# Kernel optimization log

Hardware: AMD Instinct MI355X
Metric: run time of the kernel (lower is better)

## Reference

```python
import jax, jax.numpy as jnp
import numpy as np

N = 50000      # nodes
E = 800000     # edges (before self loops)
D = 128        # embedding_dimension
HEADS = 4
C = 32         # hidden_channels
NEG_SLOPE = 0.2


def setup_inputs() -> dict:
    key = jax.random.key(0)
    ks = jax.random.split(key, 12)
    s = 0.1
    x = jax.random.normal(ks[0], (N, D), jnp.float32)
    edge_index = jax.random.randint(ks[1], (2, E), 0, N)
    # layer 1: D -> HEADS*C, concat
    W1 = jax.random.normal(ks[2], (D, HEADS * C), jnp.float32) * s
    a_src1 = jax.random.normal(ks[3], (HEADS, C), jnp.float32) * s
    a_dst1 = jax.random.normal(ks[4], (HEADS, C), jnp.float32) * s
    b1 = jnp.zeros((HEADS * C,), jnp.float32)
    # layer 2: HEADS*C -> HEADS*C, concat
    W2 = jax.random.normal(ks[5], (HEADS * C, HEADS * C), jnp.float32) * s
    a_src2 = jax.random.normal(ks[6], (HEADS, C), jnp.float32) * s
    a_dst2 = jax.random.normal(ks[7], (HEADS, C), jnp.float32) * s
    b2 = jnp.zeros((HEADS * C,), jnp.float32)
    # layer 3: HEADS*C -> C, heads=1, no concat (mean over the single head)
    W3 = jax.random.normal(ks[8], (HEADS * C, C), jnp.float32) * s
    a_src3 = jax.random.normal(ks[9], (1, C), jnp.float32) * s
    a_dst3 = jax.random.normal(ks[10], (1, C), jnp.float32) * s
    b3 = jnp.zeros((C,), jnp.float32)
    return {"x": x, "edge_index": edge_index,
            "W1": W1, "a_src1": a_src1, "a_dst1": a_dst1, "b1": b1,
            "W2": W2, "a_src2": a_src2, "a_dst2": a_dst2, "b2": b2,
            "W3": W3, "a_src3": a_src3, "a_dst3": a_dst3, "b3": b3}


def gat_layer(x, src, dst, W, a_s, a_d, b, heads, concat):
    """One PyG-style GATConv (eval mode: dropout inactive).
    x: [N, Fin]; src/dst: [E2] (self loops included)."""
    n = x.shape[0]
    h = (x @ W).reshape(n, heads, -1)                 # [N, H, C]
    alpha_src = (h * a_s).sum(-1)                     # [N, H]
    alpha_dst = (h * a_d).sum(-1)                     # [N, H]
    logits = jax.nn.leaky_relu(alpha_src[src] + alpha_dst[dst], NEG_SLOPE)  # [E2, H]
    # segment softmax over destination nodes
    m = jax.ops.segment_max(logits, dst, num_segments=n)          # [N, H]
    ex = jnp.exp(logits - m[dst])                                  # [E2, H]
    denom = jax.ops.segment_sum(ex, dst, num_segments=n)          # [N, H]
    alpha = ex / (denom[dst] + 1e-16)                              # [E2, H]
    msg = h[src] * alpha[:, :, None]                               # [E2, H, C]
    out = jax.ops.segment_sum(msg, dst, num_segments=n)            # [N, H, C]
    if concat:
        return out.reshape(n, -1) + b
    return out.mean(axis=1) + b


def reference(x, edge_index, W1, a_src1, a_dst1, b1, W2, a_src2, a_dst2, b2,
              W3, a_src3, a_dst3, b3):
    loops = jnp.arange(N, dtype=edge_index.dtype)
    src = jnp.concatenate([edge_index[0], loops])   # add_self_loops=True
    dst = jnp.concatenate([edge_index[1], loops])
    h = gat_layer(x, src, dst, W1, a_src1, a_dst1, b1, HEADS, True)
    h = jax.nn.elu(h)
    h = gat_layer(h, src, dst, W2, a_src2, a_dst2, b2, HEADS, True)
    h = jax.nn.elu(h)
    out = gat_layer(h, src, dst, W3, a_src3, a_dst3, b3, 1, False)
    return out
```

## Files before the change

### kernel.cpp

```cpp
#include <hip/hip_runtime.h>
#include <cmath>

constexpr int NN  = 50000;
constexpr int EE  = 800000;
constexpr int E2C = EE + NN;
constexpr int DIM = 128;

constexpr int NBUCK = 256;
constexpr int BW    = 196;
constexpr int EPT   = 16;
constexpr int CH    = 256 * EPT;
constexpr int NB_B  = (E2C + CH - 1) / CH;
constexpr int CAP   = 4096;

using bf16x8 = __attribute__((ext_vector_type(8))) short;
using f32x4  = __attribute__((ext_vector_type(4))) float;

__device__ inline unsigned bf16rne(float f) {
    unsigned u = __builtin_bit_cast(unsigned, f);
    return (u + 0x7fffu + ((u >> 16) & 1u)) >> 16;
}
__device__ inline float bflo(unsigned u) { return __builtin_bit_cast(float, u << 16); }
__device__ inline float bfhi(unsigned u) { return __builtin_bit_cast(float, u & 0xffff0000u); }

__global__ __launch_bounds__(256) void cvt_weights(
    const float* __restrict__ W1, const float* __restrict__ W2,
    const float* __restrict__ W3,
    unsigned short* __restrict__ W1t, unsigned short* __restrict__ W2t,
    unsigned short* __restrict__ W3t)
{
    int g = blockIdx.x * 256 + threadIdx.x;
    const float* W; unsigned short* Wt; int cols;
    if (g < 2048)      { W = W1; Wt = W1t; cols = 128; }
    else if (g < 4096) { W = W2; Wt = W2t; cols = 128; g -= 2048; }
    else if (g < 4608) { W = W3; Wt = W3t; cols = 32;  g -= 4096; }
    else return;
    int c  = g / 16;
    int k8 = (g % 16) * 8;
    unsigned up[4];
    #pragma unroll
    for (int j = 0; j < 4; ++j) {
        float a = W[(k8 + 2 * j) * cols + c];
        float b = W[(k8 + 2 * j + 1) * cols + c];
        up[j] = bf16rne(a) | (bf16rne(b) << 16);
    }
    uint4 u; u.x = up[0]; u.y = up[1]; u.z = up[2]; u.w = up[3];
    *(uint4*)(Wt + c * 128 + k8) = u;
}

template<int NT, int NH, bool F32IN>
__global__ __launch_bounds__(256) void gemm_mfma(
    const void* __restrict__ inv, const unsigned short* __restrict__ Wt,
    const float* __restrict__ a_s, const float* __restrict__ a_d,
    unsigned short* __restrict__ hout, float* __restrict__ asrc,
    float* __restrict__ adst)
{
    constexpr int COLS = NT * 16;
    constexpr int TPH  = NT / NH;
    const int lane = threadIdx.x & 63;
    const int wave = threadIdx.x >> 6;
    const int m    = lane & 15;
    const int quad = lane >> 4;
    const int n0   = blockIdx.x * 64 + wave * 16;

    int arow = n0 + m; if (arow >= NN) arow = NN - 1;

    f32x4 acc[NT] = {};
    #pragma unroll
    for (int kq = 0; kq < 4; ++kq) {
        bf16x8 a;
        if constexpr (F32IN) {
            const float* ap = (const float*)inv + (long long)arow * 128 + quad * 8 + kq * 32;
            float4 v0 = *(const float4*)ap;
            float4 v1 = *(const float4*)(ap + 4);
            a[0] = (short)bf16rne(v0.x); a[1] = (short)bf16rne(v0.y);
            a[2] = (short)bf16rne(v0.z); a[3] = (short)bf16rne(v0.w);
            a[4] = (short)bf16rne(v1.x); a[5] = (short)bf16rne(v1.y);
            a[6] = (short)bf16rne(v1.z); a[7] = (short)bf16rne(v1.w);
        } else {
            a = *(const bf16x8*)((const unsigned short*)inv
                    + (long long)arow * 128 + quad * 8 + kq * 32);
        }
        #pragma unroll
        for (int t = 0; t < NT; ++t) {
            bf16x8 b = *(const bf16x8*)(Wt + (t * 16 + m) * 128 + kq * 32 + quad * 8);
            acc[t] = __builtin_amdgcn_mfma_f32_16x16x32_bf16(a, b, acc[t], 0, 0, 0);
        }
    }

    #pragma unroll
    for (int r = 0; r < 4; ++r) {
        int node = n0 + quad * 4 + r;
        if (node < NN) {
            #pragma unroll
            for (int t = 0; t < NT; ++t)
                hout[(long long)node * COLS + t * 16 + m] =
                    (unsigned short)bf16rne(acc[t][r]);
        }
    }

    float asv[NT], adv[NT];
    #pragma unroll
    for (int t = 0; t < NT; ++t) { asv[t] = a_s[t * 16 + m]; adv[t] = a_d[t * 16 + m]; }

    #pragma unroll
    for (int r = 0; r < 4; ++r) {
        const int node = n0 + quad * 4 + r;
        #pragma unroll
        for (int hh = 0; hh < NH; ++hh) {
            float ps = 0.f, pd = 0.f;
            #pragma unroll
            for (int q = 0; q < TPH; ++q) {
                int t = hh * TPH + q;
                ps = fmaf(acc[t][r], asv[t], ps);
                pd = fmaf(acc[t][r], adv[t], pd);
            }
            #pragma unroll
            for (int off = 8; off > 0; off >>= 1) {
                ps += __shfl_down(ps, off, 16);
                pd += __shfl_down(pd, off, 16);
            }
            if (m == 0 && node < NN) {
                asrc[node * NH + hh] = ps;
                adst[node * NH + hh] = pd;
            }
        }
    }

    if (blockIdx.x == 0 && threadIdx.x == 0) {
        #pragma unroll
        for (int hh = 0; hh < NH; ++hh) asrc[NN * NH + hh] = -1e30f;
    }
}

__global__ __launch_bounds__(256) void bucket_bin(
    const int* __restrict__ ei, int* __restrict__ bcursor,
    unsigned* __restrict__ pairs)
{
    __shared__ int cnt[NBUCK];
    __shared__ int scanex[NBUCK];
    __shared__ int base[NBUCK];
    __shared__ int cur[NBUCK];
    __shared__ unsigned stage[CH];

    const int tid = threadIdx.x;
    const long long e0 = (long long)blockIdx.x * CH;
    cnt[tid] = 0;
    __syncthreads();

    unsigned rec[EPT]; int bk[EPT];
    #pragma unroll
    for (int j = 0; j < EPT; ++j) {
        long long e = e0 + tid + j * 256;
        bool valid = e < E2C;
        int ss = 0, dd = 0;
        if (valid) {
            if (e < EE) { ss = ei[e]; dd = ei[EE + e]; }
            else        { ss = dd = (int)(e - EE); }
        }
        int b = dd / BW;
        bk[j]  = valid ? b : -1;
        rec[j] = (unsigned)ss | ((unsigned)(dd - b * BW) << 16) | ((unsigned)b << 24);
        if (valid) atomicAdd(&cnt[b], 1);
    }
    __syncthreads();

    const int myc = cnt[tid];
    scanex[tid] = myc;
    __syncthreads();
    for (int off = 1; off < NBUCK; off <<= 1) {
        int t = (tid >= off) ? scanex[tid - off] : 0;
        __syncthreads();
        scanex[tid] += t;
        __syncthreads();
    }
    int excl = scanex[tid] - myc;
    __syncthreads();
    scanex[tid] = excl;
    cur[tid]    = excl;
    base[tid]   = atomicAdd(&bcursor[tid], myc);
    __syncthreads();

    #pragma unroll
    for (int j = 0; j < EPT; ++j) {
        if (bk[j] >= 0) {
            int p = atomicAdd(&cur[bk[j]], 1);
            stage[p] = rec[j];
        }
    }
    __syncthreads();

    const int total = (e0 + CH <= E2C) ? CH : (int)(E2C - e0);
    for (int j = tid; j < total; j += 256) {
        unsigned p = stage[j];
        int b = (int)(p >> 24);
        pairs[(size_t)b * CAP + base[b] + (j - scanex[b])] = p;
    }
}

__global__ __launch_bounds__(256) void bucket_sort(
    const int* __restrict__ bcursor, const unsigned* __restrict__ pairs,
    int* __restrict__ rowptr, unsigned short* __restrict__ sorted_src)
{
    __shared__ int deg[256];
    __shared__ int cur[256];
    __shared__ int gsc[256];
    const int b  = blockIdx.x;
    const int n0 = b * BW;
    const int n1 = (n0 + BW < NN) ? n0 + BW : NN;
    const int nloc = n1 - n0;
    const int tid = threadIdx.x;

    int cb = bcursor[tid];
    gsc[tid] = cb;
    __syncthreads();
    for (int off = 1; off < NBUCK; off <<= 1) {
        int t = (tid >= off) ? gsc[tid - off] : 0;
        __syncthreads();
        gsc[tid] += t;
        __syncthreads();
    }
    const int mycnt = bcursor[b];
    const int beg   = gsc[b] - mycnt;
    const unsigned* seg = pairs + (size_t)b * CAP;

    deg[tid] = 0;
    __syncthreads();
    for (int i = tid; i < mycnt; i += 256)
        atomicAdd(&deg[(seg[i] >> 16) & 0xff], 1);
    __syncthreads();

    int v = deg[tid];
    cur[tid] = v;
    __syncthreads();
    for (int off = 1; off < 256; off <<= 1) {
        int t = (tid >= off) ? cur[tid - off] : 0;
        __syncthreads();
        cur[tid] += t;
        __syncthreads();
    }
    int excl = cur[tid] - v;
    __syncthreads();
    cur[tid] = beg + excl;
    if (tid < nloc) rowptr[n0 + tid] = beg + excl;
    if (b == NBUCK - 1 && tid == 0) rowptr[NN] = E2C;
    __syncthreads();

    for (int i = tid; i < mycnt; i += 256) {
        unsigned p = seg[i];
        int pos = atomicAdd(&cur[(p >> 16) & 0xff], 1);
        sorted_src[pos] = (unsigned short)(p & 0xffff);
    }
}

template<int COLS, int NH, bool DO_ELU, bool OUTBF>
__global__ __launch_bounds__(256) void aggr_csr(
    const int* __restrict__ rowptr, const unsigned short* __restrict__ sorted_src,
    const unsigned short* __restrict__ hin,
    const float* __restrict__ asrc, const float* __restrict__ adst,
    const float* __restrict__ bias, void* __restrict__ outv)
{
    constexpr int TPN = COLS / 8;
    constexpr int USTR = COLS / 2;
    int t = blockIdx.x * 256 + threadIdx.x;
    int d = t / TPN;
    int lc = t % TPN;
    if (d >= NN) return;
    const int cc = lc * 8;
    const int head = cc / 32;
    const float ad = adst[d * NH + head];
    const int beg = rowptr[d], end = rowptr[d + 1];
    const uint* hp = (const uint*)hin + cc / 2;

    float num[8] = {};
    float den = 0.f;

    for (int i = beg; i < end; i += 4) {
        int   s[4];
        float a[4];
        uint4 Hv[4];
        #pragma unroll
        for (int j = 0; j < 4; ++j) {
            int sv = sorted_src[i + j];
            s[j] = (i + j < end) ? sv : NN;
        }
        #pragma unroll
        for (int j = 0; j < 4; ++j) a[j] = asrc[s[j] * NH + head];
        #pragma unroll
        for (int j = 0; j < 4; ++j)
            Hv[j] = *(const uint4*)&hp[(long long)s[j] * USTR];
        #pragma unroll
        for (int j = 0; j < 4; ++j) {
            float l = a[j] + ad; l = l > 0.f ? l : 0.2f * l;
            float w = __builtin_expf(l);
            den += w;
            num[0] = fmaf(w, bflo(Hv[j].x), num[0]); num[1] = fmaf(w, bfhi(Hv[j].x), num[1]);
            num[2] = fmaf(w, bflo(Hv[j].y), num[2]); num[3] = fmaf(w, bfhi(Hv[j].y), num[3]);
            num[4] = fmaf(w, bflo(Hv[j].z), num[4]); num[5] = fmaf(w, bfhi(Hv[j].z), num[5]);
            num[6] = fmaf(w, bflo(Hv[j].w), num[6]); num[7] = fmaf(w, bfhi(Hv[j].w), num[7]);
        }
    }

    float inv = 1.f / (den + 1e-16f);
    float v[8];
    #pragma unroll
    for (int j = 0; j < 8; ++j) {
        v[j] = num[j] * inv + bias[cc + j];
        if (DO_ELU) v[j] = v[j] > 0.f ? v[j] : expm1f(v[j]);
    }
    if constexpr (OUTBF) {
        uint4 u;
        u.x = bf16rne(v[0]) | (bf16rne(v[1]) << 16);
        u.y = bf16rne(v[2]) | (bf16rne(v[3]) << 16);
        u.z = bf16rne(v[4]) | (bf16rne(v[5]) << 16);
        u.w = bf16rne(v[6]) | (bf16rne(v[7]) << 16);
        *(uint4*)((unsigned short*)outv + (long long)d * COLS + cc) = u;
    } else {
        float4 o0 = {v[0], v[1], v[2], v[3]};
        float4 o1 = {v[4], v[5], v[6], v[7]};
        float* out = (float*)outv;
        *(float4*)&out[(long long)d * COLS + cc]     = o0;
        *(float4*)&out[(long long)d * COLS + cc + 4] = o1;
    }
}

extern "C" void kernel_launch(void* const* d_in, const int* in_sizes, int n_in,
                              void* d_out, int out_size, void* d_ws, size_t ws_size,
                              hipStream_t stream)
{
    const float* x   = (const float*)d_in[0];
    const int*   ei  = (const int*)  d_in[1];
    const float* W1  = (const float*)d_in[2];
    const float* as1 = (const float*)d_in[3];
    const float* ad1 = (const float*)d_in[4];
    const float* b1  = (const float*)d_in[5];
    const float* W2  = (const float*)d_in[6];
    const float* as2 = (const float*)d_in[7];
    const float* ad2 = (const float*)d_in[8];
    const float* b2  = (const float*)d_in[9];
    const float* W3  = (const float*)d_in[10];
    const float* as3 = (const float*)d_in[11];
    const float* ad3 = (const float*)d_in[12];
    const float* b3  = (const float*)d_in[13];
    float* out = (float*)d_out;

    unsigned short* H16 = (unsigned short*)d_ws;
    unsigned short* O16 = H16 + (size_t)(NN + 1) * 128;
    unsigned short* P16 = O16 + (size_t)NN * 128;
    unsigned short* W1t = P16 + (size_t)NN * 128;
    unsigned short* W2t = W1t + 128 * 128;
    unsigned short* W3t = W2t + 128 * 128;
    float* ASRC = (float*)(W3t + 32 * 128);
    float* ADST = ASRC + (size_t)(NN + 1) * 4;
    int* rowptr = (int*)(ADST + (size_t)NN * 4);
    unsigned short* sorted = (unsigned short*)(rowptr + NN + 1);
    int* bcursor = (int*)(sorted + E2C + 8);
    size_t off = ((size_t)(bcursor + NBUCK) - (size_t)d_ws + 15) & ~(size_t)15;
    unsigned* pairs = (unsigned*)((char*)d_ws + off);

    const int gCvtW    = (4608 + 255) / 256;
    const int gGemm    = (NN + 63) / 64;
    const int gAggr128 = (NN * 16 + 255) / 256;
    const int gAggr32  = (NN * 4 + 255) / 256;

    hipMemsetAsync(bcursor, 0, NBUCK * sizeof(int), stream);
    bucket_bin<<<NB_B, 256, 0, stream>>>(ei, bcursor, pairs);
    bucket_sort<<<NBUCK, 256, 0, stream>>>(bcursor, pairs, rowptr, sorted);
    cvt_weights<<<gCvtW, 256, 0, stream>>>(W1, W2, W3, W1t, W2t, W3t);

    gemm_mfma<8, 4, true><<<gGemm, 256, 0, stream>>>(x, W1t, as1, ad1, H16, ASRC, ADST);
    aggr_csr<128, 4, true, true><<<gAggr128, 256, 0, stream>>>(
        rowptr, sorted, H16, ASRC, ADST, b1, O16);

    gemm_mfma<8, 4, false><<<gGemm, 256, 0, stream>>>(O16, W2t, as2, ad2, H16, ASRC, ADST);
    aggr_csr<128, 4, true, true><<<gAggr128, 256, 0, stream>>>(
        rowptr, sorted, H16, ASRC, ADST, b2, P16);

    gemm_mfma<2, 1, false><<<gGemm, 256, 0, stream>>>(P16, W3t, as3, ad3, H16, ASRC, ADST);
    aggr_csr<32, 1, false, false><<<gAggr32, 256, 0, stream>>>(
        rowptr, sorted, H16, ASRC, ADST, b3, out);
}
```

Measured before the change: 291.7 us.

## Pad per-node CSR segments to multiples of four and prefetch source indices

Measured after the change: 277.0 us. -5.0%, faster.

```diff
diff --git a/kernel.cpp b/kernel.cpp
--- a/kernel.cpp
+++ b/kernel.cpp
@@ -12,6 +12,7 @@
 constexpr int CH    = 256 * EPT;
 constexpr int NB_B  = (E2C + CH - 1) / CH;
 constexpr int CAP   = 4096;
+constexpr int SCAP  = 5120;
 
 using bf16x8 = __attribute__((ext_vector_type(8))) short;
 using f32x4  = __attribute__((ext_vector_type(4))) float;
@@ -200,29 +201,19 @@
 
 __global__ __launch_bounds__(256) void bucket_sort(
     const int* __restrict__ bcursor, const unsigned* __restrict__ pairs,
-    int* __restrict__ rowptr, unsigned short* __restrict__ sorted_src)
+    int2* __restrict__ rowp, unsigned short* __restrict__ sorted_src)
 {
     __shared__ int deg[256];
+    __shared__ int scn[256];
     __shared__ int cur[256];
-    __shared__ int gsc[256];
     const int b  = blockIdx.x;
     const int n0 = b * BW;
     const int n1 = (n0 + BW < NN) ? n0 + BW : NN;
     const int nloc = n1 - n0;
     const int tid = threadIdx.x;
-
-    int cb = bcursor[tid];
-    gsc[tid] = cb;
-    __syncthreads();
-    for (int off = 1; off < NBUCK; off <<= 1) {
-        int t = (tid >= off) ? gsc[tid - off] : 0;
-        __syncthreads();
-        gsc[tid] += t;
-        __syncthreads();
-    }
     const int mycnt = bcursor[b];
-    const int beg   = gsc[b] - mycnt;
     const unsigned* seg = pairs + (size_t)b * CAP;
+    const int base = b * SCAP;
 
     deg[tid] = 0;
     __syncthreads();
@@ -230,22 +221,24 @@
         atomicAdd(&deg[(seg[i] >> 16) & 0xff], 1);
     __syncthreads();
 
-    int v = deg[tid];
-    cur[tid] = v;
+    const int pv = (deg[tid] + 3) & ~3;
+    scn[tid] = pv;
     __syncthreads();
     for (int off = 1; off < 256; off <<= 1) {
-        int t = (tid >= off) ? cur[tid - off] : 0;
+        int t = (tid >= off) ? scn[tid - off] : 0;
         __syncthreads();
-        cur[tid] += t;
+        scn[tid] += t;
         __syncthreads();
     }
-    int excl = cur[tid] - v;
-    __syncthreads();
-    cur[tid] = beg + excl;
-    if (tid < nloc) rowptr[n0 + tid] = beg + excl;
-    if (b == NBUCK - 1 && tid == 0) rowptr[NN] = E2C;
-    __syncthreads();
-
+    const int totalp = scn[255];
+    const int pexcl  = scn[tid] - pv;
+    cur[tid] = base + pexcl;
+    if (tid < nloc) rowp[n0 + tid] = make_int2(base + pexcl, base + pexcl + pv);
+    __syncthreads();
+
+    for (int i = tid; i < totalp; i += 256)
+        sorted_src[base + i] = (unsigned short)NN;
+    __syncthreads();
     for (int i = tid; i < mycnt; i += 256) {
         unsigned p = seg[i];
         int pos = atomicAdd(&cur[(p >> 16) & 0xff], 1);
@@ -255,7 +248,7 @@
 
 template<int COLS, int NH, bool DO_ELU, bool OUTBF>
 __global__ __launch_bounds__(256) void aggr_csr(
-    const int* __restrict__ rowptr, const unsigned short* __restrict__ sorted_src,
+    const int2* __restrict__ rowp, const unsigned short* __restrict__ sorted_src,
     const unsigned short* __restrict__ hin,
     const float* __restrict__ asrc, const float* __restrict__ adst,
     const float* __restrict__ bias, void* __restrict__ outv)
@@ -269,21 +262,19 @@
     const int cc = lc * 8;
     const int head = cc / 32;
     const float ad = adst[d * NH + head];
-    const int beg = rowptr[d], end = rowptr[d + 1];
+    const int2 be = rowp[d];
+    const int beg = be.x, end = be.y;
     const uint* hp = (const uint*)hin + cc / 2;
 
     float num[8] = {};
     float den = 0.f;
 
+    ushort4 sv = *(const ushort4*)&sorted_src[beg];
     for (int i = beg; i < end; i += 4) {
-        int   s[4];
+        ushort4 nx = *(const ushort4*)&sorted_src[i + 4];
+        const int s[4] = {sv.x, sv.y, sv.z, sv.w};
         float a[4];
         uint4 Hv[4];
-        #pragma unroll
-        for (int j = 0; j < 4; ++j) {
-            int sv = sorted_src[i + j];
-            s[j] = (i + j < end) ? sv : NN;
-        }
         #pragma unroll
         for (int j = 0; j < 4; ++j) a[j] = asrc[s[j] * NH + head];
         #pragma unroll
@@ -299,6 +290,7 @@
             num[4] = fmaf(w, bflo(Hv[j].z), num[4]); num[5] = fmaf(w, bfhi(Hv[j].z), num[5]);
             num[6] = fmaf(w, bflo(Hv[j].w), num[6]); num[7] = fmaf(w, bfhi(Hv[j].w), num[7]);
         }
+        sv = nx;
     }
 
     float inv = 1.f / (den + 1e-16f);
@@ -352,9 +344,9 @@
     unsigned short* W3t = W2t + 128 * 128;
     float* ASRC = (float*)(W3t + 32 * 128);
     float* ADST = ASRC + (size_t)(NN + 1) * 4;
-    int* rowptr = (int*)(ADST + (size_t)NN * 4);
-    unsigned short* sorted = (unsigned short*)(rowptr + NN + 1);
-    int* bcursor = (int*)(sorted + E2C + 8);
+    int2* rowp  = (int2*)(ADST + (size_t)NN * 4);
+    unsigned short* sorted = (unsigned short*)(rowp + NN);
+    int* bcursor = (int*)(sorted + (size_t)NBUCK * SCAP + 8);
     size_t off = ((size_t)(bcursor + NBUCK) - (size_t)d_ws + 15) & ~(size_t)15;
     unsigned* pairs = (unsigned*)((char*)d_ws + off);
 
@@ -365,18 +357,18 @@
 
     hipMemsetAsync(bcursor, 0, NBUCK * sizeof(int), stream);
     bucket_bin<<<NB_B, 256, 0, stream>>>(ei, bcursor, pairs);
-    bucket_sort<<<NBUCK, 256, 0, stream>>>(bcursor, pairs, rowptr, sorted);
+    bucket_sort<<<NBUCK, 256, 0, stream>>>(bcursor, pairs, rowp, sorted);
     cvt_weights<<<gCvtW, 256, 0, stream>>>(W1, W2, W3, W1t, W2t, W3t);
 
     gemm_mfma<8, 4, true><<<gGemm, 256, 0, stream>>>(x, W1t, as1, ad1, H16, ASRC, ADST);
     aggr_csr<128, 4, true, true><<<gAggr128, 256, 0, stream>>>(
-        rowptr, sorted, H16, ASRC, ADST, b1, O16);
+        rowp, sorted, H16, ASRC, ADST, b1, O16);
 
     gemm_mfma<8, 4, false><<<gGemm, 256, 0, stream>>>(O16, W2t, as2, ad2, H16, ASRC, ADST);
     aggr_csr<128, 4, true, true><<<gAggr128, 256, 0, stream>>>(
-        rowptr, sorted, H16, ASRC, ADST, b2, P16);
+        rowp, sorted, H16, ASRC, ADST, b2, P16);
 
     gemm_mfma<2, 1, false><<<gGemm, 256, 0, stream>>>(P16, W3t, as3, ad3, H16, ASRC, ADST);
     aggr_csr<32, 1, false, false><<<gAggr32, 256, 0, stream>>>(
-        rowptr, sorted, H16, ASRC, ADST, b3, out);
-}
+        rowp, sorted, H16, ASRC, ADST, b3, out);
+}
```
